# Kernel optimization log

Hardware: AMD Instinct MI355X
Metric: run time of the kernel (lower is better)

The kernel has to match this reference:

```python
import jax, jax.numpy as jnp
import numpy as np

NUM_BLOCKS = 4      # config.num_target_blocks
SCALE_MIN = 0.15    # config.target_scale_min
SCALE_MAX = 0.2     # config.target_scale_max
ASPECT = 1.0        # config.target_aspect_ratio


def setup_inputs() -> dict:
    key = jax.random.key(0)
    k1, k2, k3 = jax.random.split(key, 3)
    batch_size, height, width = 8192, 64, 64
    seq_len = height * width
    tb = batch_size * NUM_BLOCKS
    return {
        "scales": jax.random.uniform(k1, (tb,), jnp.float32),
        "rand_tops": jax.random.uniform(k2, (tb,), jnp.float32),
        "rand_lefts": jax.random.uniform(k3, (tb,), jnp.float32),
        "batch_size": batch_size,
        "seq_len": seq_len,
        "height": height,
        "width": width,
    }


def _target_mask(scales, rand_tops, rand_lefts, batch_size, seq_len, height, width):
    # scale in [SCALE_MIN, SCALE_MAX) -> integer block area (torch .int() truncates)
    s = SCALE_MIN + scales * (SCALE_MAX - SCALE_MIN)
    area = (s * height * width).astype(jnp.int32)  # [TB]
    # block_h = clamp(int(sqrt(area / aspect)), 1, H)
    bh = jnp.clip(jnp.sqrt(area.astype(jnp.float32) / ASPECT).astype(jnp.int32), 1, height)
    # block_w = clamp(int(area / block_h), 1, W)  (torch int/int is true-div then trunc)
    bw = jnp.clip((area.astype(jnp.float32) / bh.astype(jnp.float32)).astype(jnp.int32), 1, width)
    max_tops = jnp.maximum(height - bh + 1, 1)
    max_lefts = jnp.maximum(width - bw + 1, 1)
    tops = (rand_tops * max_tops.astype(jnp.float32)).astype(jnp.int32)
    lefts = (rand_lefts * max_lefts.astype(jnp.float32)).astype(jnp.int32)
    # vectorized rectangle membership, replaces the per-block python loop
    r = jnp.arange(height, dtype=jnp.int32)[None, :]   # [1,H]
    c = jnp.arange(width, dtype=jnp.int32)[None, :]    # [1,W]
    in_row = (r >= tops[:, None]) & (r < (tops + bh)[:, None])     # [TB,H]
    in_col = (c >= lefts[:, None]) & (c < (lefts + bw)[:, None])   # [TB,W]
    block = in_row[:, :, None] & in_col[:, None, :]                # [TB,H,W]
    # row-major flatten == positions rows*width+cols; keep positions < seq_len
    block = block.reshape(block.shape[0], height * width)[:, :seq_len]
    # OR together the NUM_BLOCKS rectangles per batch element
    target = jnp.any(block.reshape(batch_size, NUM_BLOCKS, seq_len), axis=1)
    return target  # [B, seq_len] bool


def reference(scales, rand_tops, rand_lefts, batch_size, seq_len, height, width):
    target_mask = _target_mask(scales, rand_tops, rand_lefts,
                               batch_size, seq_len, height, width)
    context_mask = ~target_mask
    # ragged target_positions list -> jit-friendly padded form:
    # stable argsort puts True positions (in ascending index order) first;
    # counts[b] gives how many leading entries are valid.
    positions = jnp.argsort(~target_mask, axis=1, stable=True)
    counts = target_mask.sum(axis=1, dtype=jnp.int32)
    return context_mask, target_mask, positions, counts
```

## Files before the change

### kernel.cpp

```cpp
#include <hip/hip_runtime.h>


#define NBLK 4
#define HGT 64
#define WID 64
#define SEQ 4096
#define SKEW(a) ((a) + ((a) >> 5))

__global__ __launch_bounds__(256) void blockmask_kernel(
    const float* __restrict__ scales,
    const float* __restrict__ rand_tops,
    const float* __restrict__ rand_lefts,
    int* __restrict__ out,
    int B)
{
    __shared__ int pos_s[SEQ + (SEQ >> 5)];
    __shared__ int wsum[4];

    const int b   = blockIdx.x;
    const int tid = threadIdx.x;

    int top[NBLK], bot[NBLK];
    unsigned long long cmask[NBLK];
#pragma unroll
    for (int j = 0; j < NBLK; ++j) {
        int t = b * NBLK + j;
        float sc = scales[t];
        float s = __fadd_rn(0.15f, __fmul_rn(sc, 0.05f));
        int area = (int)__fmul_rn(__fmul_rn(s, 64.0f), 64.0f);
        int bh = (int)__fsqrt_rn((float)area);
        bh = min(max(bh, 1), HGT);
        int bw = (int)__fdiv_rn((float)area, (float)bh);
        bw = min(max(bw, 1), WID);
        int maxt = max(HGT - bh + 1, 1);
        int maxl = max(WID - bw + 1, 1);
        int tp = (int)__fmul_rn(rand_tops[t],  (float)maxt);
        int lf = (int)__fmul_rn(rand_lefts[t], (float)maxl);
        top[j] = tp; bot[j] = tp + bh;
        unsigned long long m = (bw >= 64) ? ~0ull : ((1ull << bw) - 1ull);
        cmask[j] = m << lf;
    }

    const int p0 = tid * 16;
    const int r  = p0 >> 6;
    const int c0 = p0 & 63;
    unsigned long long rm = 0ull;
#pragma unroll
    for (int j = 0; j < NBLK; ++j)
        if (r >= top[j] && r < bot[j]) rm |= cmask[j];
    const unsigned mask16 = (unsigned)(rm >> c0) & 0xffffu;
    const int cnt = __popc(mask16);

    const int lane = tid & 63;
    const int wv   = tid >> 6;
    int v = cnt;
#pragma unroll
    for (int d = 1; d < 64; d <<= 1) {
        int t = __shfl_up(v, d, 64);
        if (lane >= d) v += t;
    }
    if (lane == 63) wsum[wv] = v;
    __syncthreads();
    int waveOff = 0, total = 0;
#pragma unroll
    for (int w = 0; w < 4; ++w) {
        int ws = wsum[w];
        if (w < wv) waveOff += ws;
        total += ws;
    }
    const int base_t = waveOff + (v - cnt);

#pragma unroll
    for (int k = 0; k < 16; ++k) {
        int tpre = __popc(mask16 & ((1u << k) - 1u));
        int a_t  = base_t + tpre;
        int a_n  = total + (p0 - base_t) + (k - tpre);
        int addr = ((mask16 >> k) & 1u) ? a_t : a_n;
        pos_s[SKEW(addr)] = p0 + k;
    }

    const size_t BS = (size_t)B * SEQ;
    int4* ctx4 = (int4*)out        + (size_t)b * (SEQ / 4);
    int4* tgt4 = (int4*)(out + BS) + (size_t)b * (SEQ / 4);
#pragma unroll
    for (int g = 0; g < 4; ++g) {
        int vidx = g * 256 + tid;
        int p  = vidx * 4;
        int rr = p >> 6;
        int cc = p & 63;
        unsigned long long rmg = 0ull;
#pragma unroll
        for (int j = 0; j < NBLK; ++j)
            if (rr >= top[j] && rr < bot[j]) rmg |= cmask[j];
        int m4 = (int)((rmg >> cc) & 0xfull);
        int4 tv, cv;
        tv.x =  m4       & 1; tv.y = (m4 >> 1) & 1;
        tv.z = (m4 >> 2) & 1; tv.w = (m4 >> 3) & 1;
        cv.x = tv.x ^ 1; cv.y = tv.y ^ 1; cv.z = tv.z ^ 1; cv.w = tv.w ^ 1;
        tgt4[vidx] = tv;
        ctx4[vidx] = cv;
    }

    __syncthreads();
    int4* pout4 = (int4*)(out + 2 * BS) + (size_t)b * (SEQ / 4);
#pragma unroll
    for (int g = 0; g < 4; ++g) {
        int vidx  = g * 256 + tid;
        int slot0 = vidx * 4;
        int base  = SKEW(slot0);
        int4 pv;
        pv.x = pos_s[base + 0];
        pv.y = pos_s[base + 1];
        pv.z = pos_s[base + 2];
        pv.w = pos_s[base + 3];
        pout4[vidx] = pv;
    }

    if (tid == 0) out[3 * BS + (size_t)b] = total;
}

extern "C" void kernel_launch(void* const* d_in, const int* in_sizes, int n_in,
                              void* d_out, int out_size, void* d_ws, size_t ws_size,
                              hipStream_t stream) {
    const float* scales     = (const float*)d_in[0];
    const float* rand_tops  = (const float*)d_in[1];
    const float* rand_lefts = (const float*)d_in[2];
    int* out = (int*)d_out;
    int B = in_sizes[0] / NBLK;
    blockmask_kernel<<<B, 256, 0, stream>>>(scales, rand_tops, rand_lefts, out, B);
}
```

Baseline: 401.6 us.

## Assign one wavefront per batch row and use nontemporal stores

Each 64-lane wavefront now handles a whole batch element, so a workgroup covers four elements. This removes the block-wide __syncthreads and the shared wave-sum exchange; each lane owns one grid row and scatters 64 positions into a per-wave shared buffer. Output stores become nontemporal to reduce cache pollution on the write-only stream. The trade-off is more serial scatter work per lane, with 64 LDS writes that may hit bank conflicts.

```diff
diff --git a/kernel.cpp b/kernel.cpp
--- a/kernel.cpp
+++ b/kernel.cpp
@@ -6,19 +6,23 @@
 #define WID 64
 #define SEQ 4096
 #define SKEW(a) ((a) + ((a) >> 5))
+#define WROW (SEQ + (SEQ >> 5))
+
+typedef int v4i __attribute__((ext_vector_type(4)));
 
 __global__ __launch_bounds__(256) void blockmask_kernel(
     const float* __restrict__ scales,
     const float* __restrict__ rand_tops,
     const float* __restrict__ rand_lefts,
-    int* __restrict__ out,
-    int B)
+    int* __restrict__ out, int B)
 {
-    __shared__ int pos_s[SEQ + (SEQ >> 5)];
-    __shared__ int wsum[4];
+    __shared__ int pos_s[4 * WROW];
 
-    const int b   = blockIdx.x;
-    const int tid = threadIdx.x;
+    const int tid  = threadIdx.x;
+    const int lane = tid & 63;
+    const int wv   = tid >> 6;
+    const int b    = blockIdx.x * 4 + wv;
+    if (b >= B) return;
 
     int top[NBLK], bot[NBLK];
     unsigned long long cmask[NBLK];
@@ -41,82 +45,62 @@
         cmask[j] = m << lf;
     }
 
-    const int p0 = tid * 16;
-    const int r  = p0 >> 6;
-    const int c0 = p0 & 63;
     unsigned long long rm = 0ull;
 #pragma unroll
     for (int j = 0; j < NBLK; ++j)
-        if (r >= top[j] && r < bot[j]) rm |= cmask[j];
-    const unsigned mask16 = (unsigned)(rm >> c0) & 0xffffu;
-    const int cnt = __popc(mask16);
+        if (lane >= top[j] && lane < bot[j]) rm |= cmask[j];
+    const int cnt = __popcll(rm);
 
-    const int lane = tid & 63;
-    const int wv   = tid >> 6;
     int v = cnt;
 #pragma unroll
     for (int d = 1; d < 64; d <<= 1) {
         int t = __shfl_up(v, d, 64);
         if (lane >= d) v += t;
     }
-    if (lane == 63) wsum[wv] = v;
-    __syncthreads();
-    int waveOff = 0, total = 0;
+    const int total  = __shfl(v, 63, 64);
+    const int base_t = v - cnt;
+    const int p0     = lane * 64;
+    const int base_n = total + (p0 - base_t);
+
+    int* __restrict__ ps = pos_s + wv * WROW;
 #pragma unroll
-    for (int w = 0; w < 4; ++w) {
-        int ws = wsum[w];
-        if (w < wv) waveOff += ws;
-        total += ws;
-    }
-    const int base_t = waveOff + (v - cnt);
-
-#pragma unroll
-    for (int k = 0; k < 16; ++k) {
-        int tpre = __popc(mask16 & ((1u << k) - 1u));
-        int a_t  = base_t + tpre;
-        int a_n  = total + (p0 - base_t) + (k - tpre);
-        int addr = ((mask16 >> k) & 1u) ? a_t : a_n;
-        pos_s[SKEW(addr)] = p0 + k;
+    for (int k = 0; k < 64; ++k) {
+        int bit  = (int)((rm >> k) & 1ull);
+        int tpre = __popcll(rm & ((1ull << k) - 1ull));
+        int addr = bit ? (base_t + tpre) : (base_n + k - tpre);
+        ps[SKEW(addr)] = p0 + k;
     }
 
     const size_t BS = (size_t)B * SEQ;
-    int4* ctx4 = (int4*)out        + (size_t)b * (SEQ / 4);
-    int4* tgt4 = (int4*)(out + BS) + (size_t)b * (SEQ / 4);
+    v4i* ctx4 = (v4i*)out        + (size_t)b * (SEQ / 4);
+    v4i* tgt4 = (v4i*)(out + BS) + (size_t)b * (SEQ / 4);
 #pragma unroll
-    for (int g = 0; g < 4; ++g) {
-        int vidx = g * 256 + tid;
-        int p  = vidx * 4;
-        int rr = p >> 6;
-        int cc = p & 63;
+    for (int g = 0; g < 16; ++g) {
+        int vidx = g * 64 + lane;
+        int rr = vidx >> 4;
+        int cc = (vidx & 15) * 4;
         unsigned long long rmg = 0ull;
 #pragma unroll
         for (int j = 0; j < NBLK; ++j)
             if (rr >= top[j] && rr < bot[j]) rmg |= cmask[j];
         int m4 = (int)((rmg >> cc) & 0xfull);
-        int4 tv, cv;
-        tv.x =  m4       & 1; tv.y = (m4 >> 1) & 1;
-        tv.z = (m4 >> 2) & 1; tv.w = (m4 >> 3) & 1;
-        cv.x = tv.x ^ 1; cv.y = tv.y ^ 1; cv.z = tv.z ^ 1; cv.w = tv.w ^ 1;
-        tgt4[vidx] = tv;
-        ctx4[vidx] = cv;
+        v4i tv = { m4 & 1, (m4 >> 1) & 1, (m4 >> 2) & 1, (m4 >> 3) & 1 };
+        v4i cv = { tv.x ^ 1, tv.y ^ 1, tv.z ^ 1, tv.w ^ 1 };
+        __builtin_nontemporal_store(tv, &tgt4[vidx]);
+        __builtin_nontemporal_store(cv, &ctx4[vidx]);
     }
 
-    __syncthreads();
-    int4* pout4 = (int4*)(out + 2 * BS) + (size_t)b * (SEQ / 4);
+    v4i* pout4 = (v4i*)(out + 2 * BS) + (size_t)b * (SEQ / 4);
 #pragma unroll
-    for (int g = 0; g < 4; ++g) {
-        int vidx  = g * 256 + tid;
+    for (int g = 0; g < 16; ++g) {
+        int vidx  = g * 64 + lane;
         int slot0 = vidx * 4;
         int base  = SKEW(slot0);
-        int4 pv;
-        pv.x = pos_s[base + 0];
-        pv.y = pos_s[base + 1];
-        pv.z = pos_s[base + 2];
-        pv.w = pos_s[base + 3];
-        pout4[vidx] = pv;
+        v4i pv = { ps[base + 0], ps[base + 1], ps[base + 2], ps[base + 3] };
+        __builtin_nontemporal_store(pv, &pout4[vidx]);
     }
 
-    if (tid == 0) out[3 * BS + (size_t)b] = total;
+    if (lane == 0) out[3 * BS + (size_t)b] = total;
 }
 
 extern "C" void kernel_launch(void* const* d_in, const int* in_sizes, int n_in,
@@ -127,5 +111,5 @@
     const float* rand_lefts = (const float*)d_in[2];
     int* out = (int*)d_out;
     int B = in_sizes[0] / NBLK;
-    blockmask_kernel<<<B, 256, 0, stream>>>(scales, rand_tops, rand_lefts, out, B);
+    blockmask_kernel<<<(B + 3) / 4, 256, 0, stream>>>(scales, rand_tops, rand_lefts, out, B);
 }
```

After: 405.7 us. No clear change (+1.0%).
